# Kernel tuning notes

Hardware: AMD Instinct MI355X
Metric: run time of the kernel (lower is better)

Reference implementation:

```python
import jax, jax.numpy as jnp
import numpy as np

N, C, H, W = 4, 15, 320, 320
FEATS_OUT, KSIZE, PAD, CONV_PAD, K_RBF = 32, 11, 11, 5, 31
VMAX = 1.0


def _fft2c(x):
    # fastMRI-style centered orthonormal 2D FFT on complex array [..., H, W]
    x = jnp.fft.ifftshift(x, axes=(-2, -1))
    x = jnp.fft.fft2(x, axes=(-2, -1), norm='ortho')
    return jnp.fft.fftshift(x, axes=(-2, -1))


def _ifft2c(x):
    x = jnp.fft.ifftshift(x, axes=(-2, -1))
    x = jnp.fft.ifft2(x, axes=(-2, -1), norm='ortho')
    return jnp.fft.fftshift(x, axes=(-2, -1))


def _to_c(x):
    return jax.lax.complex(x[..., 0], x[..., 1])


def _to_r(z):
    return jnp.stack([jnp.real(z), jnp.imag(z)], axis=-1)


def setup_inputs() -> dict:
    key = jax.random.key(0)
    ks = jax.random.split(key, 8)
    u_t = jax.random.normal(ks[0], (N, H, W, 2), dtype=jnp.float32)
    f = jax.random.normal(ks[1], (N, C, H, W, 2), dtype=jnp.float32)
    coil_sens = jax.random.normal(ks[2], (N, C, H, W, 2), dtype=jnp.float32)
    sampling_mask = (jax.random.uniform(ks[3], (N, H, W)) < 0.35).astype(jnp.float32)
    conv_kernel = jax.random.normal(ks[4], (FEATS_OUT, 1, KSIZE, KSIZE, 2), dtype=jnp.float32)
    conv_kernel = conv_kernel / np.sqrt(KSIZE * KSIZE * 2 * 1)
    conv_kernel = conv_kernel - jnp.mean(conv_kernel, axis=(1, 2, 3, 4), keepdims=True)
    x0 = jnp.linspace(-VMAX, VMAX, K_RBF, dtype=jnp.float32)
    w = jnp.broadcast_to((0.04 * x0).reshape(1, 1, 1, 1, K_RBF), (1, FEATS_OUT, 1, 1, K_RBF)).astype(jnp.float32)
    mu = x0
    sigma = jnp.array([2.0 * VMAX / (K_RBF - 1)], dtype=jnp.float32)
    lamb = jnp.array([1.0], dtype=jnp.float32)
    return {'u_t': u_t, 'f': f, 'coil_sens': coil_sens, 'sampling_mask': sampling_mask,
            'conv_kernel': conv_kernel, 'w': w, 'mu': mu, 'sigma': sigma, 'lamb': lamb}


def reference(u_t, f, coil_sens, sampling_mask, conv_kernel, w, mu, sigma, lamb):
    dn = ('NCHW', 'OIHW', 'NCHW')
    feats_out = conv_kernel.shape[0]
    k = conv_kernel.shape[2]

    # --- regularizer: reflect-pad, complex conv pair, RBF activation, transposed conv pair ---
    pad_cfg = ((0, 0), (0, 0), (PAD, PAD), (PAD, PAD))
    ur = jnp.pad(u_t[:, None, :, :, 0], pad_cfg, mode='reflect')  # [N,1,Hp,Wp]
    ui = jnp.pad(u_t[:, None, :, :, 1], pad_cfg, mode='reflect')

    def conv(x, Wk):
        return jax.lax.conv_general_dilated(x, Wk, (1, 1), [(CONV_PAD, CONV_PAD)] * 2,
                                            dimension_numbers=dn)

    u_k = conv(ur, conv_kernel[..., 0]) + conv(ui, conv_kernel[..., 1])  # [N,Co,Hp,Wp]

    # RBF activation: sum_i w_i * exp(-(x - mu_i)^2 / (2 sigma^2)), scanned over centers
    wk = jnp.transpose(w[0, :, 0, 0, :])  # [K, Co]
    inv2s2 = 1.0 / (2.0 * sigma[0] ** 2)

    def body(acc, wm):
        wi, mi = wm
        acc = acc + wi[None, :, None, None] * jnp.exp(-jnp.square(u_k - mi) * inv2s2)
        return acc, None

    f_u_k, _ = jax.lax.scan(body, jnp.zeros_like(u_k), (wk, mu))

    # conv_transpose2d(padding=CONV_PAD) == conv with flipped kernel, swapped channels, padding k-1-CONV_PAD
    tpad = k - 1 - CONV_PAD

    def convT(x, Wk):
        Wt = jnp.transpose(Wk[:, :, ::-1, ::-1], (1, 0, 2, 3))  # [I,O,k,k] -> OIHW w/ O=1
        return jax.lax.conv_general_dilated(x, Wt, (1, 1), [(tpad, tpad)] * 2,
                                            dimension_numbers=dn)

    Ru_r = convT(f_u_k, conv_kernel[..., 0])[:, 0]  # [N,Hp,Wp]
    Ru_i = convT(f_u_k, conv_kernel[..., 1])[:, 0]
    Ru = jnp.stack([Ru_r, Ru_i], axis=-1)[:, PAD:-PAD, PAD:-PAD, :] / feats_out  # [N,H,W,2]

    # --- data consistency: A^T (A u - f) (cartesian, os=False) ---
    u_c = _to_c(u_t)              # [N,H,W]
    c_c = _to_c(coil_sens)        # [N,C,H,W]
    f_c = _to_c(f)                # [N,C,H,W]
    m = sampling_mask[:, None]    # [N,1,H,W]
    Au = m * _fft2c(u_c[:, None] * c_c)
    At = jnp.sum(_ifft2c(m * (Au - f_c)) * jnp.conj(c_c), axis=1)  # [N,H,W]
    Du = _to_r(At) * lamb[0]

    return u_t - Ru - Du
```

## Files before the change

### kernel.cpp

```cpp
#include <hip/hip_runtime.h>
#include <hip/hip_bf16.h>
#include <math.h>

#define NN 4
#define CC 15
#define HH 320
#define WW 320
#define HW (HH*WW)
#define FF 32
#define KS 11
#define PADN 11
#define CPAD 5
#define HP 342
#define NK 31
#define NCB (NN*CC)
#define TABN 256

typedef short bf16x8 __attribute__((ext_vector_type(8)));
typedef float f32x4 __attribute__((ext_vector_type(4)));
typedef unsigned short u16x4 __attribute__((ext_vector_type(4)));

#define MFMA16 __builtin_amdgcn_mfma_f32_16x16x32_bf16

__device__ __forceinline__ unsigned int pack_bf(float r, float i) {
  __hip_bfloat16 hr = __float2bfloat16(r), hi = __float2bfloat16(i);
  unsigned short ur = *(unsigned short*)&hr, ui = *(unsigned short*)&hi;
  return (unsigned int)ur | ((unsigned int)ui << 16);
}
__device__ __forceinline__ unsigned short f2b(float x) {
  __hip_bfloat16 h = __float2bfloat16(x);
  return *(unsigned short*)&h;
}
__device__ __forceinline__ float b2f(unsigned short u) {
  __hip_bfloat16 h = *(__hip_bfloat16*)&u;
  return __bfloat162float(h);
}
__device__ __forceinline__ unsigned int rot16(unsigned int x) {
  return (x >> 16) | (x << 16);
}
__device__ __forceinline__ bf16x8 xf4(uint4 p, unsigned int x) {
  union { unsigned int u[4]; bf16x8 v; } t;
  t.u[0] = p.x ^ x; t.u[1] = p.y ^ x; t.u[2] = p.z ^ x; t.u[3] = p.w ^ x;
  return t.v;
}
__device__ __forceinline__ bf16x8 xr4(uint4 p, unsigned int x) {
  union { unsigned int u[4]; bf16x8 v; } t;
  t.u[0] = rot16(p.x) ^ x; t.u[1] = rot16(p.y) ^ x;
  t.u[2] = rot16(p.z) ^ x; t.u[3] = rot16(p.w) ^ x;
  return t.v;
}
__device__ __forceinline__ size_t pk_idx(int row, int col) {
  return (size_t)((row >> 4) * 20 + (col >> 4)) * 256 + (row & 15) * 16 + (col & 15);
}

__global__ void k_dft(unsigned int* __restrict__ Fpk) {
  int idx = blockIdx.x * blockDim.x + threadIdx.x;
  if (idx >= HW) return;
  int k = idx / WW, n = idx % WW;
  int prod = (k - 160) * (n - 160);
  int r = prod % 320; if (r < 0) r += 320;
  float ang = -6.283185307179586f * (float)r / 320.0f;
  const float s = 0.05590169943749474f;
  Fpk[pk_idx(k, n)] = pack_bf(cosf(ang) * s, sinf(ang) * s);
}

__global__ void k_prep(const float* __restrict__ ck, unsigned int* __restrict__ Wpk) {
  int idx = blockIdx.x * blockDim.x + threadIdx.x;
  if (idx >= 32 * 176) return;
  int o = idx / 176, kw = idx % 176;
  int ky = kw / 16, kx = kw % 16;
  unsigned int v = 0;
  if (kx <= 10) {
    const float* p = &ck[(o * 121 + ky * 11 + kx) * 2];
    v = pack_bf(p[0], p[1]);
  }
  Wpk[idx] = v;
}

__global__ void k_prep2(const float* __restrict__ ck, unsigned short* __restrict__ Wt) {
  int idx = blockIdx.x * blockDim.x + threadIdx.x;
  if (idx >= 2 * 11 * 16 * 32) return;
  int o = idx & 31;
  int ky = (idx >> 5) & 15;
  int rest = idx >> 9;
  int kx = rest % 11, ch = rest / 11;
  unsigned short v = 0;
  if (ky <= 10) v = f2b(ck[(o * 121 + ky * 11 + kx) * 2 + ch]);
  Wt[idx] = v;
}

__global__ void k_rbftab(const float* __restrict__ w, const float* __restrict__ mu,
                         const float* __restrict__ sigma, unsigned short* __restrict__ Tab) {
  int o = blockIdx.x;
  int e = threadIdx.x;
  if (e >= TABN + 1) return;
  float v = -2.0f + (float)e * (4.0f / (float)TABN);
  float sg = sigma[0];
  float nInv = -1.0f / (2.0f * sg * sg);
  float acc = 0.f;
  for (int i = 0; i < NK; i++) {
    float d = v - mu[i];
    acc += w[o * NK + i] * __expf(d * d * nInv);
  }
  Tab[o * 260 + e] = f2b(acc);
}

__global__ __launch_bounds__(256) void k_conv_rbf_mfma(
    const float* __restrict__ u_t, const unsigned int* __restrict__ Wpk,
    const unsigned short* __restrict__ Tab, unsigned short* __restrict__ fukT) {
  __shared__ unsigned int lW[32 * 180];
  __shared__ unsigned int tIn[26 * 32];
  __shared__ unsigned short tab[32 * 260];
  int n = blockIdx.z;
  int y0 = blockIdx.y * 16, x0 = blockIdx.x * 16;
  int tid = threadIdx.x;
  for (int i = tid; i < 32 * 176; i += 256)
    lW[(i / 176) * 180 + (i % 176)] = Wpk[i];
  {
    const unsigned int* Ts = (const unsigned int*)Tab;
    unsigned int* Td = (unsigned int*)tab;
    for (int i = tid; i < 32 * 130; i += 256) Td[i] = Ts[i];
  }
  for (int i = tid; i < 26 * 32; i += 256) {
    int rr = i >> 5, cc = i & 31;
    unsigned int v = 0;
    if (cc < 26) {
      int py = y0 + rr - 5, px = x0 + cc - 5;
      if (py >= 0 && py < HP && px >= 0 && px < HP) {
        int uy = py - PADN; uy = uy < 0 ? -uy : (uy >= HH ? 2 * (HH - 1) - uy : uy);
        int ux = px - PADN; ux = ux < 0 ? -ux : (ux >= WW ? 2 * (WW - 1) - ux : ux);
        const float* up = &u_t[((n * HH + uy) * WW + ux) * 2];
        v = pack_bf(up[0], up[1]);
      }
    }
    tIn[i] = v;
  }
  __syncthreads();
  int lane = tid & 63, wave = tid >> 6;
  int m16 = lane & 15, kq = lane >> 4;
  const short* lWs = (const short*)lW;
  f32x4 acc[4][2] = {};
  for (int ky = 0; ky < 11; ky++) {
    bf16x8 af0 = *(const bf16x8*)&lWs[m16 * 360 + ky * 32 + kq * 8];
    bf16x8 af1 = *(const bf16x8*)&lWs[(m16 + 16) * 360 + ky * 32 + kq * 8];
    #pragma unroll
    for (int nt = 0; nt < 4; nt++) {
      int rr = wave * 4 + nt + ky;
      int c0 = rr * 32 + m16 + kq * 4;
      union { unsigned int u[4]; bf16x8 v; } bu;
      bu.u[0] = tIn[c0]; bu.u[1] = tIn[c0 + 1];
      bu.u[2] = tIn[c0 + 2]; bu.u[3] = tIn[c0 + 3];
      acc[nt][0] = MFMA16(af0, bu.v, acc[nt][0], 0, 0, 0);
      acc[nt][1] = MFMA16(af1, bu.v, acc[nt][1], 0, 0, 0);
    }
  }
  const float tscale = (float)TABN / 4.0f;
  #pragma unroll
  for (int nt = 0; nt < 4; nt++) {
    int Y = y0 + wave * 4 + nt;
    int X = x0 + m16;
    if (Y >= HP || X >= HP) continue;
    #pragma unroll
    for (int mt = 0; mt < 2; mt++) {
      u16x4 pk;
      #pragma unroll
      for (int r = 0; r < 4; r++) {
        float v = acc[nt][mt][r];
        int o = mt * 16 + kq * 4 + r;
        float t = (v + 2.0f) * tscale;
        t = fminf(fmaxf(t, 0.0f), 255.999f);
        int i0 = (int)t;
        float fr = t - (float)i0;
        float a = b2f(tab[o * 260 + i0]);
        float bv = b2f(tab[o * 260 + i0 + 1]);
        pk[r] = f2b(a + (bv - a) * fr);
      }
      *(u16x4*)&fukT[(((size_t)n * HP + Y) * HP + X) * 32 + mt * 16 + kq * 4] = pk;
    }
  }
}

__global__ __launch_bounds__(256) void k_convT_mfma(
    const unsigned short* __restrict__ fukT, const unsigned short* __restrict__ Wt,
    float* __restrict__ Ru) {
  __shared__ unsigned short rowBuf[42 * 32];
  __shared__ float accS[16 * 67];
  int n = blockIdx.z;
  int y0 = blockIdx.y * 16, x0 = blockIdx.x * 32;
  int tid = threadIdx.x;
  int lane = tid & 63, wave = tid >> 6;
  int ch = wave >> 1, xh = wave & 1;
  int m16 = lane & 15, kq = lane >> 4;
  bf16x8 afr[11];
  #pragma unroll
  for (int kx = 0; kx < 11; kx++)
    afr[kx] = *(const bf16x8*)&Wt[((ch * 11 + kx) * 16 + m16) * 32 + kq * 8];
  for (int i = tid; i < 16 * 67; i += 256) accS[i] = 0.f;
  int xl = xh * 16 + m16;
  for (int t = 0; t < 26; t++) {
    int r = y0 + 6 + t;
    __syncthreads();
    {
      const unsigned int* src = (const unsigned int*)&fukT[(((size_t)n * HP + r) * HP + x0 + 6) * 32];
      unsigned int* dst = (unsigned int*)rowBuf;
      for (int i = tid; i < 42 * 16; i += 256) dst[i] = src[i];
    }
    __syncthreads();
    f32x4 dacc = {};
    #pragma unroll
    for (int kx = 0; kx < 11; kx++) {
      bf16x8 bfrag = *(const bf16x8*)&rowBuf[(xl + 10 - kx) * 32 + kq * 8];
      dacc = MFMA16(afr[kx], bfrag, dacc, 0, 0, 0);
    }
    #pragma unroll
    for (int rg = 0; rg < 4; rg++) {
      int ky = kq * 4 + rg;
      int y = t + ky - 10;
      if (ky <= 10 && y >= 0 && y < 16)
        accS[y * 67 + xl * 2 + ch] += dacc[rg];
    }
  }
  __syncthreads();
  int chO = tid & 1, xO = (tid >> 1) & 31, yb = tid >> 6;
  #pragma unroll
  for (int q = 0; q < 4; q++) {
    int y = yb + q * 4;
    Ru[(((size_t)n * HH + y0 + y) * WW + x0 + xO) * 2 + chO] = accS[y * 67 + xO * 2 + chO];
  }
}

__global__ __launch_bounds__(256) void k_umulT(const float* __restrict__ u_t,
                                               const float* __restrict__ cs,
                                               unsigned int* __restrict__ X0T) {
  __shared__ unsigned int t[32 * 33];
  int bc = blockIdx.x;
  int b = blockIdx.y;
  int n = b / CC;
  int ty = (bc / 10) * 32, tx = (bc % 10) * 32;
  int r = threadIdx.x >> 5, c = threadIdx.x & 31;
  #pragma unroll
  for (int q = 0; q < 4; q++) {
    int y = ty + r + q * 8, x = tx + c;
    const float* up = &u_t[((size_t)n * HW + (size_t)y * WW + x) * 2];
    const float* cp = &cs[((size_t)b * HW + (size_t)y * WW + x) * 2];
    float ur = up[0], ui = up[1], crr = cp[0], cii = cp[1];
    t[(r + q * 8) * 33 + c] = pack_bf(ur * crr - ui * cii, ur * cii + ui * crr);
  }
  __syncthreads();
  #pragma unroll
  for (int q = 0; q < 4; q++) {
    int xx = r + q * 8;
    int x = tx + xx, y = ty + c;
    X0T[(size_t)b * HW + pk_idx(x, y)] = t[c * 33 + xx];
  }
}

template <int MODE>
__global__ __launch_bounds__(512, 4) void k_dcpair(
    const unsigned int* __restrict__ Fpk,
    const unsigned int* __restrict__ Bp,
    const float* __restrict__ mask, const float* __restrict__ fdat,
    unsigned int* __restrict__ Out) {
  __shared__ unsigned int sMem[32 * 340];
  int bid = blockIdx.x;
  int wg = (bid & 7) * 75 + (bid >> 3);
  int b = wg / 10, strip = wg % 10;
  int i0 = strip * 32;
  int tid = threadIdx.x;
  int lane = tid & 63, wave = tid >> 6;
  int wr = wave >> 2, wc = wave & 3;
  int m16 = lane & 15, kq = lane >> 4;
  int loff = m16 * 16 + kq * 4;
  const unsigned int XA1 = (MODE == 1) ? 0x80000000u : 0u;
  const unsigned int XA2 = (MODE == 1) ? 0u : 0x00008000u;

  const unsigned int* Ap = Fpk + (size_t)(strip * 2 + wr) * 5120 + loff;
  const unsigned int* Bb = Bp + (size_t)b * HW + (size_t)(wc * 5) * 5120 + loff;
  f32x4 aR[5] = {}, aI[5] = {};
  uint4 ap = *(const uint4*)&Ap[0];
  uint4 bp[5];
  #pragma unroll
  for (int ct = 0; ct < 5; ct++) bp[ct] = *(const uint4*)&Bb[ct * 5120];
  #pragma unroll
  for (int kc = 0; kc < 20; kc++) {
    bf16x8 a1 = xf4(ap, XA1), a2 = xr4(ap, XA2);
    bf16x8 bcur[5];
    #pragma unroll
    for (int ct = 0; ct < 5; ct++) bcur[ct] = *(const bf16x8*)&bp[ct];
    if (kc < 19) {
      ap = *(const uint4*)&Ap[(kc + 1) * 256];
      #pragma unroll
      for (int ct = 0; ct < 5; ct++)
        bp[ct] = *(const uint4*)&Bb[ct * 5120 + (kc + 1) * 256];
    }
    #pragma unroll
    for (int ct = 0; ct < 5; ct++) {
      aR[ct] = MFMA16(a1, bcur[ct], aR[ct], 0, 0, 0);
      aI[ct] = MFMA16(a2, bcur[ct], aI[ct], 0, 0, 0);
    }
  }
  #pragma unroll
  for (int ct = 0; ct < 5; ct++)
    #pragma unroll
    for (int r = 0; r < 4; r++) {
      int trow = wr * 16 + kq * 4 + r;
      int tcol = wc * 80 + ct * 16 + m16;
      unsigned int v = pack_bf(aR[ct][r], aI[ct][r]);
      if (MODE == 2) v ^= 0x80000000u;
      sMem[trow * 340 + tcol] = v;
    }
  __syncthreads();

  f32x4 cR[5] = {}, cI[5] = {};
  const unsigned int* Tr = &sMem[(wr * 16 + m16) * 340];
  const unsigned int* Fb = Fpk + (size_t)(wc * 5) * 5120 + loff;
  uint4 tp = *(const uint4*)&Tr[kq * 4];
  uint4 fp[5];
  #pragma unroll
  for (int ct = 0; ct < 5; ct++) fp[ct] = *(const uint4*)&Fb[ct * 5120];
  #pragma unroll
  for (int kc = 0; kc < 20; kc++) {
    bf16x8 a1 = xf4(tp, 0x80000000u), a2 = xr4(tp, 0u);
    bf16x8 bcur[5];
    #pragma unroll
    for (int ct = 0; ct < 5; ct++) bcur[ct] = *(const bf16x8*)&fp[ct];
    if (kc < 19) {
      tp = *(const uint4*)&Tr[(kc + 1) * 16 + kq * 4];
      #pragma unroll
      for (int ct = 0; ct < 5; ct++)
        fp[ct] = *(const uint4*)&Fb[ct * 5120 + (kc + 1) * 256];
    }
    #pragma unroll
    for (int ct = 0; ct < 5; ct++) {
      cR[ct] = MFMA16(a1, bcur[ct], cR[ct], 0, 0, 0);
      cI[ct] = MFMA16(a2, bcur[ct], cI[ct], 0, 0, 0);
    }
  }

  if constexpr (MODE == 1) {
    __syncthreads();
    int n = b / CC;
    #pragma unroll
    for (int ct = 0; ct < 5; ct++)
      #pragma unroll
      for (int r = 0; r < 4; r++) {
        int row = i0 + wr * 16 + kq * 4 + r;
        int col = wc * 80 + ct * 16 + m16;
        float m = mask[n * HW + row * WW + col];
        size_t fi = ((size_t)b * HW + (size_t)row * WW + col) * 2;
        float vr = m * (cR[ct][r] - fdat[fi]);
        float vi = m * (cI[ct][r] - fdat[fi + 1]);
        sMem[col * 33 + (row - i0)] = pack_bf(vr, vi);
      }
    __syncthreads();
    for (int i2 = tid; i2 < 320 * 32; i2 += 512) {
      int x = i2 >> 5, yy = i2 & 31;
      Out[(size_t)b * HW + pk_idx(x, i0 + yy)] = sMem[x * 33 + yy];
    }
  } else {
    #pragma unroll
    for (int ct = 0; ct < 5; ct++)
      #pragma unroll
      for (int r = 0; r < 4; r++) {
        int row = i0 + wr * 16 + kq * 4 + r;
        int col = wc * 80 + ct * 16 + m16;
        Out[(size_t)b * HW + (size_t)row * WW + col] =
            pack_bf(cR[ct][r], cI[ct][r]) ^ 0x80000000u;
      }
  }
}

__global__ void k_coilsum(const unsigned int* __restrict__ Z, const float* __restrict__ cs,
                          float* __restrict__ At) {
  int idx = blockIdx.x * blockDim.x + threadIdx.x;
  if (idx >= NN * HW) return;
  int n = idx / HW, hw = idx % HW;
  float ar = 0.f, ai = 0.f;
  for (int c = 0; c < CC; c++) {
    size_t zi = (size_t)(n * CC + c) * HW + hw;
    unsigned int p = Z[zi];
    float zr = b2f((unsigned short)(p & 0xffff));
    float zim = b2f((unsigned short)(p >> 16));
    float crr = cs[zi * 2], cii = cs[zi * 2 + 1];
    ar += zr * crr + zim * cii;
    ai += zim * crr - zr * cii;
  }
  At[idx * 2] = ar;
  At[idx * 2 + 1] = ai;
}

__global__ void k_final(const float* __restrict__ u_t, const float* __restrict__ Ru,
                        const float* __restrict__ At, const float* __restrict__ lamb,
                        float* __restrict__ out) {
  int idx = blockIdx.x * blockDim.x + threadIdx.x;
  if (idx >= NN * HW * 2) return;
  out[idx] = u_t[idx] - Ru[idx] * (1.0f / (float)FF) - lamb[0] * At[idx];
}

extern "C" void kernel_launch(void* const* d_in, const int* in_sizes, int n_in,
                              void* d_out, int out_size, void* d_ws, size_t ws_size,
                              hipStream_t stream) {
  const float* u_t   = (const float*)d_in[0];
  const float* fdat  = (const float*)d_in[1];
  const float* cs    = (const float*)d_in[2];
  const float* mask  = (const float*)d_in[3];
  const float* ck    = (const float*)d_in[4];
  const float* w     = (const float*)d_in[5];
  const float* mu    = (const float*)d_in[6];
  const float* sigma = (const float*)d_in[7];
  const float* lamb  = (const float*)d_in[8];
  float* out = (float*)d_out;

  unsigned int* wsw = (unsigned int*)d_ws;
  unsigned int* Fpk = wsw;
  unsigned int* Wpk = wsw + 102400;
  unsigned short* Wt = (unsigned short*)(wsw + 108160);
  unsigned short* Tab = (unsigned short*)(wsw + 113792);
  float* At = (float*)(wsw + 117952);
  float* Ru = (float*)(wsw + 937152);
  unsigned int* big = wsw + 1756352;
  unsigned short* fukT = (unsigned short*)big;
  unsigned int* X0T = big;
  unsigned int* P2T = big + 6144000;
  unsigned int* Q = big;

  k_dft<<<(HW + 255) / 256, 256, 0, stream>>>(Fpk);
  k_prep<<<(32 * 176 + 255) / 256, 256, 0, stream>>>(ck, Wpk);
  k_prep2<<<(2 * 11 * 16 * 32 + 255) / 256, 256, 0, stream>>>(ck, Wt);
  k_rbftab<<<32, 320, 0, stream>>>(w, mu, sigma, Tab);
  k_conv_rbf_mfma<<<dim3(22, 22, NN), 256, 0, stream>>>(u_t, Wpk, Tab, fukT);
  k_convT_mfma<<<dim3(10, 20, NN), 256, 0, stream>>>(fukT, Wt, Ru);
  k_umulT<<<dim3(100, 60), 256, 0, stream>>>(u_t, cs, X0T);
  k_dcpair<1><<<600, 512, 0, stream>>>(Fpk, X0T, mask, fdat, P2T);
  k_dcpair<2><<<600, 512, 0, stream>>>(Fpk, P2T, nullptr, nullptr, Q);
  k_coilsum<<<(NN * HW + 255) / 256, 256, 0, stream>>>(Q, cs, At);
  k_final<<<(NN * HW * 2 + 255) / 256, 256, 0, stream>>>(u_t, Ru, At, lamb, out);
}
```

Before: 425.8 us.

## Halve dcpair row strip to 16 rows and double-buffer first GEMM loads

The DFT-pair kernel now processes 16-row strips with 256-thread blocks (4 waves, one row of waves), launching twice as many blocks, with shared memory cut to match. The first GEMM stage uses two register buffers to prefetch two k-steps ahead instead of one. The intent is to raise occupancy and parallelism and hide global-load latency better. In exchange, the shared B and F operand tiles are reused across fewer rows per block, which raises global/L2 traffic, and register pressure goes up.

```diff
diff --git a/kernel.cpp b/kernel.cpp
--- a/kernel.cpp
+++ b/kernel.cpp
@@ -256,54 +256,79 @@
 }
 
 template <int MODE>
-__global__ __launch_bounds__(512, 4) void k_dcpair(
+__global__ __launch_bounds__(256, 4) void k_dcpair(
     const unsigned int* __restrict__ Fpk,
     const unsigned int* __restrict__ Bp,
     const float* __restrict__ mask, const float* __restrict__ fdat,
     unsigned int* __restrict__ Out) {
-  __shared__ unsigned int sMem[32 * 340];
+  __shared__ unsigned int sMem[5440];
   int bid = blockIdx.x;
-  int wg = (bid & 7) * 75 + (bid >> 3);
-  int b = wg / 10, strip = wg % 10;
-  int i0 = strip * 32;
+  int wg = (bid & 7) * 150 + (bid >> 3);
+  int b = wg / 20, strip = wg % 20;
+  int i0 = strip * 16;
   int tid = threadIdx.x;
-  int lane = tid & 63, wave = tid >> 6;
-  int wr = wave >> 2, wc = wave & 3;
+  int lane = tid & 63, wc = tid >> 6;
   int m16 = lane & 15, kq = lane >> 4;
   int loff = m16 * 16 + kq * 4;
   const unsigned int XA1 = (MODE == 1) ? 0x80000000u : 0u;
   const unsigned int XA2 = (MODE == 1) ? 0u : 0x00008000u;
 
-  const unsigned int* Ap = Fpk + (size_t)(strip * 2 + wr) * 5120 + loff;
+  const unsigned int* Ap = Fpk + (size_t)strip * 5120 + loff;
   const unsigned int* Bb = Bp + (size_t)b * HW + (size_t)(wc * 5) * 5120 + loff;
+
   f32x4 aR[5] = {}, aI[5] = {};
-  uint4 ap = *(const uint4*)&Ap[0];
-  uint4 bp[5];
-  #pragma unroll
-  for (int ct = 0; ct < 5; ct++) bp[ct] = *(const uint4*)&Bb[ct * 5120];
-  #pragma unroll
-  for (int kc = 0; kc < 20; kc++) {
-    bf16x8 a1 = xf4(ap, XA1), a2 = xr4(ap, XA2);
-    bf16x8 bcur[5];
-    #pragma unroll
-    for (int ct = 0; ct < 5; ct++) bcur[ct] = *(const bf16x8*)&bp[ct];
-    if (kc < 19) {
-      ap = *(const uint4*)&Ap[(kc + 1) * 256];
-      #pragma unroll
-      for (int ct = 0; ct < 5; ct++)
-        bp[ct] = *(const uint4*)&Bb[ct * 5120 + (kc + 1) * 256];
-    }
-    #pragma unroll
-    for (int ct = 0; ct < 5; ct++) {
-      aR[ct] = MFMA16(a1, bcur[ct], aR[ct], 0, 0, 0);
-      aI[ct] = MFMA16(a2, bcur[ct], aI[ct], 0, 0, 0);
+  uint4 a0 = *(const uint4*)&Ap[0];
+  uint4 a1v = *(const uint4*)&Ap[256];
+  uint4 b0[5], b1[5];
+  #pragma unroll
+  for (int ct = 0; ct < 5; ct++) {
+    b0[ct] = *(const uint4*)&Bb[ct * 5120];
+    b1[ct] = *(const uint4*)&Bb[ct * 5120 + 256];
+  }
+  #pragma unroll
+  for (int kc2 = 0; kc2 < 10; kc2++) {
+    {
+      const int kc = kc2 * 2;
+      bf16x8 x1 = xf4(a0, XA1), x2 = xr4(a0, XA2);
+      bf16x8 bc[5];
+      #pragma unroll
+      for (int ct = 0; ct < 5; ct++) bc[ct] = *(const bf16x8*)&b0[ct];
+      if (kc + 2 < 20) {
+        a0 = *(const uint4*)&Ap[(kc + 2) * 256];
+        #pragma unroll
+        for (int ct = 0; ct < 5; ct++)
+          b0[ct] = *(const uint4*)&Bb[ct * 5120 + (kc + 2) * 256];
+      }
+      #pragma unroll
+      for (int ct = 0; ct < 5; ct++) {
+        aR[ct] = MFMA16(x1, bc[ct], aR[ct], 0, 0, 0);
+        aI[ct] = MFMA16(x2, bc[ct], aI[ct], 0, 0, 0);
+      }
+    }
+    {
+      const int kc = kc2 * 2 + 1;
+      bf16x8 x1 = xf4(a1v, XA1), x2 = xr4(a1v, XA2);
+      bf16x8 bc[5];
+      #pragma unroll
+      for (int ct = 0; ct < 5; ct++) bc[ct] = *(const bf16x8*)&b1[ct];
+      if (kc + 2 < 20) {
+        a1v = *(const uint4*)&Ap[(kc + 2) * 256];
+        #pragma unroll
+        for (int ct = 0; ct < 5; ct++)
+          b1[ct] = *(const uint4*)&Bb[ct * 5120 + (kc + 2) * 256];
+      }
+      #pragma unroll
+      for (int ct = 0; ct < 5; ct++) {
+        aR[ct] = MFMA16(x1, bc[ct], aR[ct], 0, 0, 0);
+        aI[ct] = MFMA16(x2, bc[ct], aI[ct], 0, 0, 0);
+      }
     }
   }
   #pragma unroll
   for (int ct = 0; ct < 5; ct++)
     #pragma unroll
     for (int r = 0; r < 4; r++) {
-      int trow = wr * 16 + kq * 4 + r;
+      int trow = kq * 4 + r;
       int tcol = wc * 80 + ct * 16 + m16;
       unsigned int v = pack_bf(aR[ct][r], aI[ct][r]);
       if (MODE == 2) v ^= 0x80000000u;
@@ -312,7 +337,7 @@
   __syncthreads();
 
   f32x4 cR[5] = {}, cI[5] = {};
-  const unsigned int* Tr = &sMem[(wr * 16 + m16) * 340];
+  const unsigned int* Tr = &sMem[m16 * 340];
   const unsigned int* Fb = Fpk + (size_t)(wc * 5) * 5120 + loff;
   uint4 tp = *(const uint4*)&Tr[kq * 4];
   uint4 fp[5];
@@ -320,10 +345,10 @@
   for (int ct = 0; ct < 5; ct++) fp[ct] = *(const uint4*)&Fb[ct * 5120];
   #pragma unroll
   for (int kc = 0; kc < 20; kc++) {
-    bf16x8 a1 = xf4(tp, 0x80000000u), a2 = xr4(tp, 0u);
-    bf16x8 bcur[5];
-    #pragma unroll
-    for (int ct = 0; ct < 5; ct++) bcur[ct] = *(const bf16x8*)&fp[ct];
+    bf16x8 x1 = xf4(tp, 0x80000000u), x2 = xr4(tp, 0u);
+    bf16x8 bc[5];
+    #pragma unroll
+    for (int ct = 0; ct < 5; ct++) bc[ct] = *(const bf16x8*)&fp[ct];
     if (kc < 19) {
       tp = *(const uint4*)&Tr[(kc + 1) * 16 + kq * 4];
       #pragma unroll
@@ -332,8 +357,8 @@
     }
     #pragma unroll
     for (int ct = 0; ct < 5; ct++) {
-      cR[ct] = MFMA16(a1, bcur[ct], cR[ct], 0, 0, 0);
-      cI[ct] = MFMA16(a2, bcur[ct], cI[ct], 0, 0, 0);
+      cR[ct] = MFMA16(x1, bc[ct], cR[ct], 0, 0, 0);
+      cI[ct] = MFMA16(x2, bc[ct], cI[ct], 0, 0, 0);
     }
   }
 
@@ -344,25 +369,25 @@
     for (int ct = 0; ct < 5; ct++)
       #pragma unroll
       for (int r = 0; r < 4; r++) {
-        int row = i0 + wr * 16 + kq * 4 + r;
+        int row = i0 + kq * 4 + r;
         int col = wc * 80 + ct * 16 + m16;
         float m = mask[n * HW + row * WW + col];
         size_t fi = ((size_t)b * HW + (size_t)row * WW + col) * 2;
         float vr = m * (cR[ct][r] - fdat[fi]);
         float vi = m * (cI[ct][r] - fdat[fi + 1]);
-        sMem[col * 33 + (row - i0)] = pack_bf(vr, vi);
+        sMem[col * 17 + kq * 4 + r] = pack_bf(vr, vi);
       }
     __syncthreads();
-    for (int i2 = tid; i2 < 320 * 32; i2 += 512) {
-      int x = i2 >> 5, yy = i2 & 31;
-      Out[(size_t)b * HW + pk_idx(x, i0 + yy)] = sMem[x * 33 + yy];
+    for (int i2 = tid; i2 < 320 * 16; i2 += 256) {
+      int x = i2 >> 4, yy = i2 & 15;
+      Out[(size_t)b * HW + pk_idx(x, i0 + yy)] = sMem[x * 17 + yy];
     }
   } else {
     #pragma unroll
     for (int ct = 0; ct < 5; ct++)
       #pragma unroll
       for (int r = 0; r < 4; r++) {
-        int row = i0 + wr * 16 + kq * 4 + r;
+        int row = i0 + kq * 4 + r;
         int col = wc * 80 + ct * 16 + m16;
         Out[(size_t)b * HW + (size_t)row * WW + col] =
             pack_bf(cR[ct][r], cI[ct][r]) ^ 0x80000000u;
@@ -431,8 +456,8 @@
   k_conv_rbf_mfma<<<dim3(22, 22, NN), 256, 0, stream>>>(u_t, Wpk, Tab, fukT);
   k_convT_mfma<<<dim3(10, 20, NN), 256, 0, stream>>>(fukT, Wt, Ru);
   k_umulT<<<dim3(100, 60), 256, 0, stream>>>(u_t, cs, X0T);
-  k_dcpair<1><<<600, 512, 0, stream>>>(Fpk, X0T, mask, fdat, P2T);
-  k_dcpair<2><<<600, 512, 0, stream>>>(Fpk, P2T, nullptr, nullptr, Q);
+  k_dcpair<1><<<1200, 256, 0, stream>>>(Fpk, X0T, mask, fdat, P2T);
+  k_dcpair<2><<<1200, 256, 0, stream>>>(Fpk, P2T, nullptr, nullptr, Q);
   k_coilsum<<<(NN * HW + 255) / 256, 256, 0, stream>>>(Q, cs, At);
   k_final<<<(NN * HW * 2 + 255) / 256, 256, 0, stream>>>(u_t, Ru, At, lamb, out);
 }
```

Result: no change. 424.1 us (-0.4%).

## Stage DFT operands through LDS with async global_load_lds ring buffer and swizzle

Applied to the files above, without the earlier changes.

Rewrites the paired DFT-matmul kernel so that each block uses 4 waves, with each wave computing two row tiles. The B operand (input or DFT matrix) is streamed into a 4-deep LDS ring using direct global-to-LDS loads and explicit vmcnt waits, and the DFT strip is staged in LDS once. The packed tile layout gains an XOR swizzle to avoid LDS bank conflicts, and the mode-1 output is now written directly in packed, swizzled form, which removes the transpose pass through shared memory. The aim is to cut redundant global reads and hide load latency behind MFMA work. The cost is larger LDS use (about 120KB per block) and lower occupancy.

```diff
diff --git a/kernel.cpp b/kernel.cpp
--- a/kernel.cpp
+++ b/kernel.cpp
@@ -49,8 +49,13 @@
   t.u[2] = rot16(p.z) ^ x; t.u[3] = rot16(p.w) ^ x;
   return t.v;
 }
+__device__ __forceinline__ int swzw(int w) {
+  int c = w >> 2;
+  c ^= (c >> 3) & 7;
+  return (c << 2) | (w & 3);
+}
 __device__ __forceinline__ size_t pk_idx(int row, int col) {
-  return (size_t)((row >> 4) * 20 + (col >> 4)) * 256 + (row & 15) * 16 + (col & 15);
+  return (size_t)((row >> 4) * 20 + (col >> 4)) * 256 + swzw((row & 15) * 16 + (col & 15));
 }
 
 __global__ void k_dft(unsigned int* __restrict__ Fpk) {
@@ -255,117 +260,165 @@
   }
 }
 
+#define BUF4(i) ((i) == 0 ? sB0 : ((i) == 1 ? sB1 : ((i) == 2 ? sB2 : sB3)))
+
 template <int MODE>
-__global__ __launch_bounds__(512, 4) void k_dcpair(
+__global__ __launch_bounds__(256, 2) void k_dcpair(
     const unsigned int* __restrict__ Fpk,
     const unsigned int* __restrict__ Bp,
     const float* __restrict__ mask, const float* __restrict__ fdat,
     unsigned int* __restrict__ Out) {
-  __shared__ unsigned int sMem[32 * 340];
+  __shared__ unsigned int sA[10240];
+  __shared__ unsigned int sB0[5120], sB1[5120], sB2[5120], sB3[5120];
   int bid = blockIdx.x;
   int wg = (bid & 7) * 75 + (bid >> 3);
   int b = wg / 10, strip = wg % 10;
   int i0 = strip * 32;
   int tid = threadIdx.x;
-  int lane = tid & 63, wave = tid >> 6;
-  int wr = wave >> 2, wc = wave & 3;
+  int lane = tid & 63, wc = tid >> 6;
   int m16 = lane & 15, kq = lane >> 4;
   int loff = m16 * 16 + kq * 4;
+  int loffS = swzw(loff);
   const unsigned int XA1 = (MODE == 1) ? 0x80000000u : 0u;
   const unsigned int XA2 = (MODE == 1) ? 0u : 0x00008000u;
 
-  const unsigned int* Ap = Fpk + (size_t)(strip * 2 + wr) * 5120 + loff;
-  const unsigned int* Bb = Bp + (size_t)b * HW + (size_t)(wc * 5) * 5120 + loff;
-  f32x4 aR[5] = {}, aI[5] = {};
-  uint4 ap = *(const uint4*)&Ap[0];
-  uint4 bp[5];
-  #pragma unroll
-  for (int ct = 0; ct < 5; ct++) bp[ct] = *(const uint4*)&Bb[ct * 5120];
-  #pragma unroll
-  for (int kc = 0; kc < 20; kc++) {
-    bf16x8 a1 = xf4(ap, XA1), a2 = xr4(ap, XA2);
-    bf16x8 bcur[5];
-    #pragma unroll
-    for (int ct = 0; ct < 5; ct++) bcur[ct] = *(const bf16x8*)&bp[ct];
-    if (kc < 19) {
-      ap = *(const uint4*)&Ap[(kc + 1) * 256];
+  const unsigned int* Astrip = Fpk + (size_t)strip * 10240;
+  const unsigned int* Bb = Bp + (size_t)b * HW + (size_t)(wc * 5) * 5120;
+  const unsigned int* Fb = Fpk + (size_t)(wc * 5) * 5120;
+
+  #pragma unroll
+  for (int f = 0; f < 10; f++)
+    __builtin_amdgcn_global_load_lds(Astrip + (wc * 10 + f) * 256 + lane * 4,
+                                     &sA[(wc * 10 + f) * 256], 16, 0, 0);
+  #pragma unroll
+  for (int ct = 0; ct < 5; ct++)
+    __builtin_amdgcn_global_load_lds(Bb + ct * 5120 + lane * 4,
+                                     &sB0[(wc * 5 + ct) * 256], 16, 0, 0);
+  #pragma unroll
+  for (int ct = 0; ct < 5; ct++)
+    __builtin_amdgcn_global_load_lds(Bb + ct * 5120 + 256 + lane * 4,
+                                     &sB1[(wc * 5 + ct) * 256], 16, 0, 0);
+  __syncthreads();
+
+  f32x4 aR0[5] = {}, aI0[5] = {}, aR1[5] = {}, aI1[5] = {};
+  #pragma unroll
+  for (int kf = 0; kf < 20; kf++) {
+    const unsigned int* rdb = BUF4(kf & 3);
+    if (kf < 18) {
+      unsigned int* stb = BUF4((kf + 2) & 3);
       #pragma unroll
       for (int ct = 0; ct < 5; ct++)
-        bp[ct] = *(const uint4*)&Bb[ct * 5120 + (kc + 1) * 256];
-    }
+        __builtin_amdgcn_global_load_lds(Bb + ct * 5120 + (kf + 2) * 256 + lane * 4,
+                                         &stb[(wc * 5 + ct) * 256], 16, 0, 0);
+      asm volatile("s_waitcnt vmcnt(10)" ::: "memory");
+    } else if (kf == 18) {
+      asm volatile("s_waitcnt vmcnt(5)" ::: "memory");
+    } else {
+      asm volatile("s_waitcnt vmcnt(0)" ::: "memory");
+    }
+    uint4 a0 = *(const uint4*)&sA[kf * 256 + loffS];
+    uint4 a1 = *(const uint4*)&sA[5120 + kf * 256 + loffS];
+    bf16x8 x10 = xf4(a0, XA1), x20 = xr4(a0, XA2);
+    bf16x8 x11 = xf4(a1, XA1), x21 = xr4(a1, XA2);
     #pragma unroll
     for (int ct = 0; ct < 5; ct++) {
-      aR[ct] = MFMA16(a1, bcur[ct], aR[ct], 0, 0, 0);
-      aI[ct] = MFMA16(a2, bcur[ct], aI[ct], 0, 0, 0);
-    }
-  }
+      uint4 bq = *(const uint4*)&rdb[(wc * 5 + ct) * 256 + loffS];
+      bf16x8 bb = *(const bf16x8*)&bq;
+      aR0[ct] = MFMA16(x10, bb, aR0[ct], 0, 0, 0);
+      aI0[ct] = MFMA16(x20, bb, aI0[ct], 0, 0, 0);
+      aR1[ct] = MFMA16(x11, bb, aR1[ct], 0, 0, 0);
+      aI1[ct] = MFMA16(x21, bb, aI1[ct], 0, 0, 0);
+    }
+  }
+
+  __syncthreads();
   #pragma unroll
   for (int ct = 0; ct < 5; ct++)
     #pragma unroll
     for (int r = 0; r < 4; r++) {
-      int trow = wr * 16 + kq * 4 + r;
-      int tcol = wc * 80 + ct * 16 + m16;
-      unsigned int v = pack_bf(aR[ct][r], aI[ct][r]);
-      if (MODE == 2) v ^= 0x80000000u;
-      sMem[trow * 340 + tcol] = v;
-    }
-  __syncthreads();
-
-  f32x4 cR[5] = {}, cI[5] = {};
-  const unsigned int* Tr = &sMem[(wr * 16 + m16) * 340];
-  const unsigned int* Fb = Fpk + (size_t)(wc * 5) * 5120 + loff;
-  uint4 tp = *(const uint4*)&Tr[kq * 4];
-  uint4 fp[5];
-  #pragma unroll
-  for (int ct = 0; ct < 5; ct++) fp[ct] = *(const uint4*)&Fb[ct * 5120];
-  #pragma unroll
-  for (int kc = 0; kc < 20; kc++) {
-    bf16x8 a1 = xf4(tp, 0x80000000u), a2 = xr4(tp, 0u);
-    bf16x8 bcur[5];
-    #pragma unroll
-    for (int ct = 0; ct < 5; ct++) bcur[ct] = *(const bf16x8*)&fp[ct];
-    if (kc < 19) {
-      tp = *(const uint4*)&Tr[(kc + 1) * 16 + kq * 4];
+      unsigned int v0 = pack_bf(aR0[ct][r], aI0[ct][r]);
+      unsigned int v1 = pack_bf(aR1[ct][r], aI1[ct][r]);
+      if (MODE == 2) { v0 ^= 0x80000000u; v1 ^= 0x80000000u; }
+      int w = swzw((kq * 4 + r) * 16 + m16);
+      sA[(wc * 5 + ct) * 256 + w] = v0;
+      sA[(20 + wc * 5 + ct) * 256 + w] = v1;
+    }
+  #pragma unroll
+  for (int ct = 0; ct < 5; ct++)
+    __builtin_amdgcn_global_load_lds(Fb + ct * 5120 + lane * 4,
+                                     &sB0[(wc * 5 + ct) * 256], 16, 0, 0);
+  #pragma unroll
+  for (int ct = 0; ct < 5; ct++)
+    __builtin_amdgcn_global_load_lds(Fb + ct * 5120 + 256 + lane * 4,
+                                     &sB1[(wc * 5 + ct) * 256], 16, 0, 0);
+  __syncthreads();
+
+  f32x4 cR0[5] = {}, cI0[5] = {}, cR1[5] = {}, cI1[5] = {};
+  #pragma unroll
+  for (int kf = 0; kf < 20; kf++) {
+    const unsigned int* rdb = BUF4(kf & 3);
+    if (kf < 18) {
+      unsigned int* stb = BUF4((kf + 2) & 3);
       #pragma unroll
       for (int ct = 0; ct < 5; ct++)
-        fp[ct] = *(const uint4*)&Fb[ct * 5120 + (kc + 1) * 256];
-    }
+        __builtin_amdgcn_global_load_lds(Fb + ct * 5120 + (kf + 2) * 256 + lane * 4,
+                                         &stb[(wc * 5 + ct) * 256], 16, 0, 0);
+      asm volatile("s_waitcnt vmcnt(10)" ::: "memory");
+    } else if (kf == 18) {
+      asm volatile("s_waitcnt vmcnt(5)" ::: "memory");
+    } else {
+      asm volatile("s_waitcnt vmcnt(0)" ::: "memory");
+    }
+    uint4 t0 = *(const uint4*)&sA[kf * 256 + loffS];
+    uint4 t1 = *(const uint4*)&sA[5120 + kf * 256 + loffS];
+    bf16x8 x10 = xf4(t0, 0x80000000u), x20 = xr4(t0, 0u);
+    bf16x8 x11 = xf4(t1, 0x80000000u), x21 = xr4(t1, 0u);
     #pragma unroll
     for (int ct = 0; ct < 5; ct++) {
-      cR[ct] = MFMA16(a1, bcur[ct], cR[ct], 0, 0, 0);
-      cI[ct] = MFMA16(a2, bcur[ct], cI[ct], 0, 0, 0);
+      uint4 bq = *(const uint4*)&rdb[(wc * 5 + ct) * 256 + loffS];
+      bf16x8 bb = *(const bf16x8*)&bq;
+      cR0[ct] = MFMA16(x10, bb, cR0[ct], 0, 0, 0);
+      cI0[ct] = MFMA16(x20, bb, cI0[ct], 0, 0, 0);
+      cR1[ct] = MFMA16(x11, bb, cR1[ct], 0, 0, 0);
+      cI1[ct] = MFMA16(x21, bb, cI1[ct], 0, 0, 0);
     }
   }
 
   if constexpr (MODE == 1) {
-    __syncthreads();
     int n = b / CC;
+    #pragma unroll
+    for (int ct = 0; ct < 5; ct++) {
+      int col = wc * 80 + ct * 16 + m16;
+      uint4 s0, s1;
+      #pragma unroll
+      for (int r = 0; r < 4; r++) {
+        int row0 = i0 + kq * 4 + r;
+        float m0 = mask[n * HW + row0 * WW + col];
+        size_t f0i = ((size_t)b * HW + (size_t)row0 * WW + col) * 2;
+        ((unsigned int*)&s0)[r] =
+            pack_bf(m0 * (cR0[ct][r] - fdat[f0i]), m0 * (cI0[ct][r] - fdat[f0i + 1]));
+        int row1 = row0 + 16;
+        float m1 = mask[n * HW + row1 * WW + col];
+        size_t f1i = ((size_t)b * HW + (size_t)row1 * WW + col) * 2;
+        ((unsigned int*)&s1)[r] =
+            pack_bf(m1 * (cR1[ct][r] - fdat[f1i]), m1 * (cI1[ct][r] - fdat[f1i + 1]));
+      }
+      size_t base = (size_t)b * HW + (size_t)((wc * 5 + ct) * 20 + strip * 2) * 256 + loffS;
+      *(uint4*)&Out[base] = s0;
+      *(uint4*)&Out[base + 256] = s1;
+    }
+  } else {
     #pragma unroll
     for (int ct = 0; ct < 5; ct++)
       #pragma unroll
       for (int r = 0; r < 4; r++) {
-        int row = i0 + wr * 16 + kq * 4 + r;
         int col = wc * 80 + ct * 16 + m16;
-        float m = mask[n * HW + row * WW + col];
-        size_t fi = ((size_t)b * HW + (size_t)row * WW + col) * 2;
-        float vr = m * (cR[ct][r] - fdat[fi]);
-        float vi = m * (cI[ct][r] - fdat[fi + 1]);
-        sMem[col * 33 + (row - i0)] = pack_bf(vr, vi);
-      }
-    __syncthreads();
-    for (int i2 = tid; i2 < 320 * 32; i2 += 512) {
-      int x = i2 >> 5, yy = i2 & 31;
-      Out[(size_t)b * HW + pk_idx(x, i0 + yy)] = sMem[x * 33 + yy];
-    }
-  } else {
-    #pragma unroll
-    for (int ct = 0; ct < 5; ct++)
-      #pragma unroll
-      for (int r = 0; r < 4; r++) {
-        int row = i0 + wr * 16 + kq * 4 + r;
-        int col = wc * 80 + ct * 16 + m16;
-        Out[(size_t)b * HW + (size_t)row * WW + col] =
-            pack_bf(cR[ct][r], cI[ct][r]) ^ 0x80000000u;
+        int row0 = i0 + kq * 4 + r;
+        int row1 = i0 + 16 + kq * 4 + r;
+        Out[(size_t)b * HW + (size_t)row0 * WW + col] =
+            pack_bf(cR0[ct][r], cI0[ct][r]) ^ 0x80000000u;
+        Out[(size_t)b * HW + (size_t)row1 * WW + col] =
+            pack_bf(cR1[ct][r], cI1[ct][r]) ^ 0x80000000u;
       }
   }
 }
@@ -431,8 +484,8 @@
   k_conv_rbf_mfma<<<dim3(22, 22, NN), 256, 0, stream>>>(u_t, Wpk, Tab, fukT);
   k_convT_mfma<<<dim3(10, 20, NN), 256, 0, stream>>>(fukT, Wt, Ru);
   k_umulT<<<dim3(100, 60), 256, 0, stream>>>(u_t, cs, X0T);
-  k_dcpair<1><<<600, 512, 0, stream>>>(Fpk, X0T, mask, fdat, P2T);
-  k_dcpair<2><<<600, 512, 0, stream>>>(Fpk, P2T, nullptr, nullptr, Q);
+  k_dcpair<1><<<600, 256, 0, stream>>>(Fpk, X0T, mask, fdat, P2T);
+  k_dcpair<2><<<600, 256, 0, stream>>>(Fpk, P2T, nullptr, nullptr, Q);
   k_coilsum<<<(NN * HW + 255) / 256, 256, 0, stream>>>(Q, cs, At);
   k_final<<<(NN * HW * 2 + 255) / 256, 256, 0, stream>>>(u_t, Ru, At, lamb, out);
 }
```

Result: faster. 380.4 us (-10.7%).
